# Optimization experiments

Measured on AMD Instinct MI355X. Metric: run time of the kernel, lower is better.

Reference implementation:

```python
import jax, jax.numpy as jnp
import numpy as np

EPS = 1e-5
NHEADS = 4
NLAYERS = 6

def layernorm(x, g, b):
    m = jnp.mean(x, axis=-1, keepdims=True)
    v = jnp.var(x, axis=-1, keepdims=True)
    return (x - m) * jax.lax.rsqrt(v + EPS) * g + b

def leaky_relu(x):
    return jnp.where(x >= 0, x, 0.1 * x)  # LeakyReLU(negative_slope=0.1)

def biased_mha(x, bias, mask, Wq, bq, Wk, bk, Wv, bv, Wo, bo):
    # dgl.nn.BiasedMHA: scores = (q/sqrt(dh)) k^T + bias (per-head), mask==True -> -inf
    B, N, D = x.shape
    dh = D // NHEADS
    q = (x @ Wq + bq).reshape(B, N, NHEADS, dh) * (dh ** -0.5)
    k = (x @ Wk + bk).reshape(B, N, NHEADS, dh)
    v = (x @ Wv + bv).reshape(B, N, NHEADS, dh)
    scores = jnp.einsum('bqhd,bkhd->bqkh', q, k) + bias  # [B,N,N,H]
    scores = jnp.where(mask[..., None], -jnp.inf, scores)
    w = jax.nn.softmax(scores, axis=2)  # softmax over keys
    out = jnp.einsum('bqkh,bkhd->bqhd', w, v).reshape(B, N, D)
    return out @ Wo + bo

def graphormer_forward(node_feat_new, attn_bias, deg_in_emb, deg_out_emb,
                       mlp_n_W1, mlp_n_b1, mlp_n_W2, mlp_n_b2,
                       Wq, bq, Wk, bk, Wv, bv, Wo, bo,
                       ln1_g, ln1_b, W1, b1, W2, b2, ln2_g, ln2_b,
                       mlp_out_W1, mlp_out_b1, mlp_out_W2, mlp_out_b2,
                       in_degree, out_degree, attn_mask, po_idx):
    # DegreeEncoder (directed): clamp to max_degree=8, sum of two embedding tables
    deg = deg_in_emb[jnp.clip(in_degree, 0, 8)] + deg_out_emb[jnp.clip(out_degree, 0, 8)]
    # mlp_n: Linear -> LeakyReLU(0.1) -> Linear
    h = leaky_relu(node_feat_new @ mlp_n_W1 + mlp_n_b1) @ mlp_n_W2 + mlp_n_b2
    x = h + deg
    mask = attn_mask != 0
    for i in range(NLAYERS):  # 6 GraphormerLayers, norm_first=False (post-norm)
        res = x
        a = biased_mha(x, attn_bias, mask, Wq[i], bq[i], Wk[i], bk[i], Wv[i], bv[i], Wo[i], bo[i])
        x = layernorm(res + a, ln1_g[i], ln1_b[i])
        res = x
        f = jax.nn.relu(x @ W1[i] + b1[i]) @ W2[i] + b2[i]  # FFN with ReLU
        x = layernorm(res + f, ln2_g[i], ln2_b[i])
    B = x.shape[0]
    sel = x[jnp.arange(B)[:, None], po_idx].reshape(-1, x.shape[-1])  # gather PO nodes
    return leaky_relu(sel @ mlp_out_W1 + mlp_out_b1) @ mlp_out_W2 + mlp_out_b2

def setup_inputs():
    B, N, F_IN, D, HID, P, L = 8, 1024, 64, 512, 1024, 128, 6
    key = jax.random.key(0)
    ks = jax.random.split(key, 32)
    def w(k, shape, fan_in):
        return jax.random.normal(k, shape, jnp.float32) / np.float32(np.sqrt(fan_in))
    return dict(
        node_feat_new=jax.random.normal(ks[0], (B, N, F_IN), jnp.float32),
        in_degree=jax.random.randint(ks[1], (B, N), 0, 9),
        out_degree=jax.random.randint(ks[2], (B, N), 0, 9),
        dist=jax.random.randint(ks[3], (B, N, N), 0, 6).astype(jnp.int32),
        attn_mask=jax.random.randint(ks[4], (B, N, N), 0, 2).astype(jnp.int32),
        po_idx=jax.random.randint(ks[5], (B, P), 0, N),
        attn_bias=jax.random.uniform(ks[6], (B, N, N, NHEADS), jnp.float32),
        deg_in_emb=w(ks[7], (9, D), D),
        deg_out_emb=w(ks[8], (9, D), D),
        mlp_n_W1=w(ks[9], (F_IN, D // 2), F_IN), mlp_n_b1=jnp.zeros((D // 2,), jnp.float32),
        mlp_n_W2=w(ks[10], (D // 2, D), D // 2), mlp_n_b2=jnp.zeros((D,), jnp.float32),
        Wq=w(ks[11], (L, D, D), D), bq=jnp.zeros((L, D), jnp.float32),
        Wk=w(ks[12], (L, D, D), D), bk=jnp.zeros((L, D), jnp.float32),
        Wv=w(ks[13], (L, D, D), D), bv=jnp.zeros((L, D), jnp.float32),
        Wo=w(ks[14], (L, D, D), D), bo=jnp.zeros((L, D), jnp.float32),
        ln1_g=jnp.ones((L, D), jnp.float32), ln1_b=jnp.zeros((L, D), jnp.float32),
        W1=w(ks[15], (L, D, HID), D), b1=jnp.zeros((L, HID), jnp.float32),
        W2=w(ks[16], (L, HID, D), HID), b2=jnp.zeros((L, D), jnp.float32),
        ln2_g=jnp.ones((L, D), jnp.float32), ln2_b=jnp.zeros((L, D), jnp.float32),
        mlp_out_W1=w(ks[17], (D, D // 2), D), mlp_out_b1=jnp.zeros((D // 2,), jnp.float32),
        mlp_out_W2=w(ks[18], (D // 2, 1), D // 2), mlp_out_b2=jnp.zeros((1,), jnp.float32),
    )

def reference(node_feat_new, in_degree, out_degree, dist, attn_mask, po_idx, attn_bias,
              deg_in_emb, deg_out_emb, mlp_n_W1, mlp_n_b1, mlp_n_W2, mlp_n_b2,
              Wq, bq, Wk, bk, Wv, bv, Wo, bo, ln1_g, ln1_b, W1, b1, W2, b2, ln2_g, ln2_b,
              mlp_out_W1, mlp_out_b1, mlp_out_W2, mlp_out_b2):
    del dist  # original computes spatial encoding from dist but overwrites attn_bias with rand (dead code)
    return graphormer_forward(node_feat_new, attn_bias, deg_in_emb, deg_out_emb,
                              mlp_n_W1, mlp_n_b1, mlp_n_W2, mlp_n_b2,
                              Wq, bq, Wk, bk, Wv, bv, Wo, bo,
                              ln1_g, ln1_b, W1, b1, W2, b2, ln2_g, ln2_b,
                              mlp_out_W1, mlp_out_b1, mlp_out_W2, mlp_out_b2,
                              in_degree, out_degree, attn_mask, po_idx)
```

## Files before the change

kernel.cpp:

```cpp
#include <hip/hip_runtime.h>

typedef unsigned short u16;
typedef unsigned int u32;
typedef short bf16x8 __attribute__((ext_vector_type(8)));
typedef float f32x4 __attribute__((ext_vector_type(4)));

__device__ __forceinline__ float us2f(u16 u) {
  union { unsigned int i; float f; } x; x.i = ((unsigned int)u) << 16; return x.f;
}
__device__ __forceinline__ u16 f2bf(float f) {
  union { float f; unsigned int i; } x; x.f = f;
  unsigned int i = x.i;
  return (u16)((i + 0x7FFFu + ((i >> 16) & 1u)) >> 16);
}
__device__ __forceinline__ int probe_f32(const void* p) {
  return ((const u16*)p)[0] == 0;
}
__device__ __forceinline__ float ldf(const void* p, size_t i, int f32) {
  return f32 ? ((const float*)p)[i] : us2f(((const u16*)p)[i]);
}
__device__ __forceinline__ float4 ldf4(const void* p, size_t i, int f32) {
  if (f32) return *(const float4*)((const float*)p + i);
  const ushort4 t = *(const ushort4*)((const u16*)p + i);
  return make_float4(us2f(t.x), us2f(t.y), us2f(t.z), us2f(t.w));
}

__global__ __launch_bounds__(256) void gemm_mfma(
    const void* __restrict__ probe, const void* __restrict__ A, int a_mode,
    int lda, const void* __restrict__ W, size_t wOff,
    const void* __restrict__ bias, size_t bOff, const u16* __restrict__ res,
    void* __restrict__ C, int c_bf16, int M, int N, int K, int act) {
  const int in_f32 = probe_f32(probe);
  const int a_f32 = (a_mode == 2) ? in_f32 : 0;
  __shared__ u16 As[2][128][40];
  __shared__ u16 Bt[2][64][40];
  const int tid = threadIdx.x;
  const int n0 = blockIdx.x * 64, m0 = blockIdx.y * 128;
  const int wv = tid >> 6, lane = tid & 63;
  const int lk = lane & 15, quad = lane >> 4;
  const int wm = wv * 32;

  f32x4 acc[2][4];
#pragma unroll
  for (int i = 0; i < 2; i++)
#pragma unroll
    for (int j = 0; j < 4; j++) acc[i][j] = (f32x4){0.f, 0.f, 0.f, 0.f};

  const int sar = tid >> 1, sac = (tid & 1) * 16;
  const int kp = tid & 15, nseg = tid >> 4;

  u16 abuf[16];
  u32 wbuf[8];
  auto loadA = [&](int k0) {
    if (a_f32) {
      const float* ap = (const float*)A + (size_t)(m0 + sar) * lda + k0 + sac;
#pragma unroll
      for (int q = 0; q < 4; q++) {
        const float4 f = *(const float4*)(ap + q * 4);
        abuf[q * 4 + 0] = f2bf(f.x); abuf[q * 4 + 1] = f2bf(f.y);
        abuf[q * 4 + 2] = f2bf(f.z); abuf[q * 4 + 3] = f2bf(f.w);
      }
    } else {
      const u16* ap = (const u16*)A + (size_t)(m0 + sar) * lda + k0 + sac;
      *(bf16x8*)&abuf[0] = *(const bf16x8*)ap;
      *(bf16x8*)&abuf[8] = *(const bf16x8*)(ap + 8);
    }
  };
  auto loadW = [&](int k0) {
    if (tid < 128) {
      const size_t wb = wOff + (size_t)(k0 + 2 * kp) * N + n0 + nseg * 8;
      if (in_f32) {
        const float* wp = (const float*)W + wb;
#pragma unroll
        for (int i = 0; i < 8; i++)
          wbuf[i] = ((u32)f2bf(wp[N + i]) << 16) | (u32)f2bf(wp[i]);
      } else {
        const u16* wp = (const u16*)W + wb;
#pragma unroll
        for (int i = 0; i < 8; i++)
          wbuf[i] = ((u32)wp[N + i] << 16) | (u32)wp[i];
      }
    }
  };
  auto store = [&](int bi) {
    *(bf16x8*)&As[bi][sar][sac] = *(bf16x8*)&abuf[0];
    *(bf16x8*)&As[bi][sar][sac + 8] = *(bf16x8*)&abuf[8];
    if (tid < 128) {
#pragma unroll
      for (int i = 0; i < 8; i++) *(u32*)&Bt[bi][nseg * 8 + i][2 * kp] = wbuf[i];
    }
  };

  const int nk = K >> 5;
  loadA(0); loadW(0); store(0);
  __syncthreads();
  for (int kt = 0; kt < nk; kt++) {
    const int cur = kt & 1;
    if (kt + 1 < nk) { loadA((kt + 1) * 32); loadW((kt + 1) * 32); }
    bf16x8 af[2], bfv[4];
#pragma unroll
    for (int i = 0; i < 2; i++)
      af[i] = *(const bf16x8*)&As[cur][wm + i * 16 + lk][quad * 8];
#pragma unroll
    for (int j = 0; j < 4; j++)
      bfv[j] = *(const bf16x8*)&Bt[cur][j * 16 + lk][quad * 8];
#pragma unroll
    for (int i = 0; i < 2; i++)
#pragma unroll
      for (int j = 0; j < 4; j++)
        acc[i][j] = __builtin_amdgcn_mfma_f32_16x16x32_bf16(af[i], bfv[j],
                                                            acc[i][j], 0, 0, 0);
    if (kt + 1 < nk) store(cur ^ 1);
    __syncthreads();
  }

#pragma unroll
  for (int j = 0; j < 4; j++) {
    const int col = n0 + j * 16 + lk;
    const float bb = bias ? ldf(bias, bOff + col, in_f32) : 0.f;
#pragma unroll
    for (int i = 0; i < 2; i++) {
#pragma unroll
      for (int r = 0; r < 4; r++) {
        const int row = m0 + wm + i * 16 + quad * 4 + r;
        float t = acc[i][j][r] + bb;
        if (act == 1) t = t > 0.f ? t : 0.f;
        else if (act == 2) t = t >= 0.f ? t : 0.1f * t;
        if (res) t += us2f(res[(size_t)row * N + col]);
        if (c_bf16) ((u16*)C)[(size_t)row * N + col] = f2bf(t);
        else ((float*)C)[(size_t)row * N + col] = t;
      }
    }
  }
}

__global__ __launch_bounds__(256) void gemm_qkv(
    const void* __restrict__ probe, const u16* __restrict__ A,
    const void* __restrict__ Wq, const void* __restrict__ Wk,
    const void* __restrict__ Wv, size_t wOff, const void* __restrict__ bq,
    const void* __restrict__ bk, const void* __restrict__ bv, size_t bOff,
    u16* __restrict__ C) {
  const int in_f32 = probe_f32(probe);
  __shared__ u16 As[2][128][40];
  __shared__ u16 Bt[2][64][40];
  const int tid = threadIdx.x;
  const int n0 = blockIdx.x * 64, m0 = blockIdx.y * 128;
  const int src = n0 >> 9, nn0 = n0 & 511;
  const void* W = src == 0 ? Wq : (src == 1 ? Wk : Wv);
  const void* bias = src == 0 ? bq : (src == 1 ? bk : bv);
  const int wv = tid >> 6, lane = tid & 63;
  const int lk = lane & 15, quad = lane >> 4;
  const int wm = wv * 32;

  f32x4 acc[2][4];
#pragma unroll
  for (int i = 0; i < 2; i++)
#pragma unroll
    for (int j = 0; j < 4; j++) acc[i][j] = (f32x4){0.f, 0.f, 0.f, 0.f};

  const int sar = tid >> 1, sac = (tid & 1) * 16;
  const int kp = tid & 15, nseg = tid >> 4;

  u16 abuf[16];
  u32 wbuf[8];
  auto loadA = [&](int k0) {
    const u16* ap = A + (size_t)(m0 + sar) * 512 + k0 + sac;
    *(bf16x8*)&abuf[0] = *(const bf16x8*)ap;
    *(bf16x8*)&abuf[8] = *(const bf16x8*)(ap + 8);
  };
  auto loadW = [&](int k0) {
    if (tid < 128) {
      const size_t wb = wOff + (size_t)(k0 + 2 * kp) * 512 + nn0 + nseg * 8;
      if (in_f32) {
        const float* wp = (const float*)W + wb;
#pragma unroll
        for (int i = 0; i < 8; i++)
          wbuf[i] = ((u32)f2bf(wp[512 + i]) << 16) | (u32)f2bf(wp[i]);
      } else {
        const u16* wp = (const u16*)W + wb;
#pragma unroll
        for (int i = 0; i < 8; i++)
          wbuf[i] = ((u32)wp[512 + i] << 16) | (u32)wp[i];
      }
    }
  };
  auto store = [&](int bi) {
    *(bf16x8*)&As[bi][sar][sac] = *(bf16x8*)&abuf[0];
    *(bf16x8*)&As[bi][sar][sac + 8] = *(bf16x8*)&abuf[8];
    if (tid < 128) {
#pragma unroll
      for (int i = 0; i < 8; i++) *(u32*)&Bt[bi][nseg * 8 + i][2 * kp] = wbuf[i];
    }
  };

  loadA(0); loadW(0); store(0);
  __syncthreads();
  for (int kt = 0; kt < 16; kt++) {
    const int cur = kt & 1;
    if (kt < 15) { loadA((kt + 1) * 32); loadW((kt + 1) * 32); }
    bf16x8 af[2], bfv[4];
#pragma unroll
    for (int i = 0; i < 2; i++)
      af[i] = *(const bf16x8*)&As[cur][wm + i * 16 + lk][quad * 8];
#pragma unroll
    for (int j = 0; j < 4; j++)
      bfv[j] = *(const bf16x8*)&Bt[cur][j * 16 + lk][quad * 8];
#pragma unroll
    for (int i = 0; i < 2; i++)
#pragma unroll
      for (int j = 0; j < 4; j++)
        acc[i][j] = __builtin_amdgcn_mfma_f32_16x16x32_bf16(af[i], bfv[j],
                                                            acc[i][j], 0, 0, 0);
    if (kt < 15) store(cur ^ 1);
    __syncthreads();
  }

#pragma unroll
  for (int j = 0; j < 4; j++) {
    const int coll = nn0 + j * 16 + lk;
    const float bb = ldf(bias, bOff + coll, in_f32);
#pragma unroll
    for (int i = 0; i < 2; i++) {
#pragma unroll
      for (int r = 0; r < 4; r++) {
        const int row = m0 + wm + i * 16 + quad * 4 + r;
        C[(size_t)row * 1536 + n0 + j * 16 + lk] = f2bf(acc[i][j][r] + bb);
      }
    }
  }
}

__global__ __launch_bounds__(256) void deg_kernel(const void* __restrict__ probe,
    u16* __restrict__ x, const int* __restrict__ ind, const int* __restrict__ outd,
    const void* __restrict__ ein, const void* __restrict__ eout) {
  const int f32 = probe_f32(probe);
  const int r = blockIdx.x, tid = threadIdx.x;
  int a = ind[r]; a = a < 0 ? 0 : (a > 8 ? 8 : a);
  int b = outd[r]; b = b < 0 ? 0 : (b > 8 ? 8 : b);
  const size_t base = (size_t)r * 512;
  for (int c = tid; c < 512; c += 256) {
    const float v = us2f(x[base + c]) + ldf(ein, (size_t)a * 512 + c, f32) +
                    ldf(eout, (size_t)b * 512 + c, f32);
    x[base + c] = f2bf(v);
  }
}

__global__ __launch_bounds__(256) void bias_pack(const void* __restrict__ probe,
    const void* __restrict__ bias, const int* __restrict__ mask,
    u16* __restrict__ biasm) {
  const int f32 = probe_f32(probe);
  const int bq = blockIdx.x;
  const int k = threadIdx.x * 4;
  const size_t rk = (size_t)bq * 1024 + k;
  const int4 mv = *(const int4*)(mask + rk);
  const float4 hk0 = ldf4(bias, rk * 4, f32);
  const float4 hk1 = ldf4(bias, rk * 4 + 4, f32);
  const float4 hk2 = ldf4(bias, rk * 4 + 8, f32);
  const float4 hk3 = ldf4(bias, rk * 4 + 12, f32);
  const u16 NB = f2bf(-3.0e38f);
  const int b = bq >> 10, q = bq & 1023;
  const size_t ob = (((size_t)b * 4 * 1024) + q) * 1024 + k;
#define PACK(H, C)                                                   \
  {                                                                  \
    ushort4 p;                                                       \
    p.x = mv.x ? NB : f2bf(hk0.C); p.y = mv.y ? NB : f2bf(hk1.C);    \
    p.z = mv.z ? NB : f2bf(hk2.C); p.w = mv.w ? NB : f2bf(hk3.C);    \
    *(ushort4*)(biasm + ob + ((size_t)H << 20)) = p;                 \
  }
  PACK(0, x)
  PACK(1, y)
  PACK(2, z)
  PACK(3, w)
#undef PACK
}

__global__ __launch_bounds__(256) void attn_mfma(const void* __restrict__ probe,
    const u16* __restrict__ QKV, const void* __restrict__ bias,
    const int* __restrict__ mask, u16* __restrict__ O,
    const u16* __restrict__ biasm) {
  const int f32 = probe_f32(probe);
  __shared__ u16 Kls[2][32][136];
  __shared__ u16 Vt[2][128][40];
  __shared__ u16 Pl[4][16][40];
  const int b = blockIdx.z, h = blockIdx.y, q0 = blockIdx.x * 64;
  const int tid = threadIdx.x;
  const int wv = tid >> 6, lane = tid & 63;
  const int lk = lane & 15, quad = lane >> 4;
  const float scale = 0.08838834764831845f;
  const float NEG = -3.0e38f;

  const size_t qg = (size_t)(b * 1024 + q0 + wv * 16);
  const int lq = q0 + wv * 16;
  const u16* bm = biasm ? biasm + (((size_t)(b * 4 + h)) << 20) : (const u16*)0;

  bf16x8 qf[4];
#pragma unroll
  for (int c = 0; c < 4; c++)
    qf[c] = *(const bf16x8*)(QKV + (qg + lk) * 1536 + h * 128 + c * 32 + quad * 8);

  f32x4 o[8];
#pragma unroll
  for (int c = 0; c < 8; c++) o[c] = (f32x4){0.f, 0.f, 0.f, 0.f};
  float m_st[4], l_st[4];
#pragma unroll
  for (int r = 0; r < 4; r++) { m_st[r] = NEG; l_st[r] = 0.f; }

  const int kp = tid & 15, dseg = tid >> 4;

  bf16x8 ka, kb2, va, vb2;
  auto loadKV = [&](int k0) {
    const size_t r0 = (size_t)(b * 1024 + k0 + 2 * kp) * 1536 + h * 128 + dseg * 8;
    ka  = *(const bf16x8*)(QKV + r0 + 512);
    kb2 = *(const bf16x8*)(QKV + r0 + 512 + 1536);
    va  = *(const bf16x8*)(QKV + r0 + 1024);
    vb2 = *(const bf16x8*)(QKV + r0 + 1024 + 1536);
  };
  auto storeKV = [&](int bi) {
    *(bf16x8*)&Kls[bi][2 * kp][dseg * 8] = ka;
    *(bf16x8*)&Kls[bi][2 * kp + 1][dseg * 8] = kb2;
#pragma unroll
    for (int i = 0; i < 8; i++) {
      const unsigned int pk =
          ((unsigned int)(u16)vb2[i] << 16) | (unsigned int)(u16)va[i];
      *(unsigned int*)&Vt[bi][dseg * 8 + i][2 * kp] = pk;
    }
  };

  loadKV(0); storeKV(0);
  __syncthreads();

  for (int kt = 0; kt < 32; kt++) {
    const int cur = kt & 1;
    const int k0 = kt * 32;
    if (kt < 31) loadKV((kt + 1) * 32);

    f32x4 sa[2];
#pragma unroll
    for (int kh = 0; kh < 2; kh++) {
      sa[kh] = (f32x4){0.f, 0.f, 0.f, 0.f};
#pragma unroll
      for (int c = 0; c < 4; c++) {
        const bf16x8 kf = *(const bf16x8*)&Kls[cur][kh * 16 + lk][c * 32 + quad * 8];
        sa[kh] = __builtin_amdgcn_mfma_f32_16x16x32_bf16(qf[c], kf, sa[kh], 0, 0, 0);
      }
    }
    float sv[2][4];
    if (bm) {
#pragma unroll
      for (int kh = 0; kh < 2; kh++)
#pragma unroll
        for (int r = 0; r < 4; r++)
          sv[kh][r] = sa[kh][r] * scale +
              us2f(bm[(size_t)(lq + quad * 4 + r) * 1024 + (k0 + kh * 16 + lk)]);
    } else {
#pragma unroll
      for (int kh = 0; kh < 2; kh++)
#pragma unroll
        for (int r = 0; r < 4; r++) {
          const size_t bidx = (qg + quad * 4 + r) * 1024 + (size_t)(k0 + kh * 16 + lk);
          const float s = sa[kh][r] * scale + ldf(bias, bidx * 4 + h, f32);
          sv[kh][r] = mask[bidx] ? NEG : s;
        }
    }
#pragma unroll
    for (int r = 0; r < 4; r++) {
      float lm = fmaxf(sv[0][r], sv[1][r]);
      lm = fmaxf(lm, __shfl_xor(lm, 1));
      lm = fmaxf(lm, __shfl_xor(lm, 2));
      lm = fmaxf(lm, __shfl_xor(lm, 4));
      lm = fmaxf(lm, __shfl_xor(lm, 8));
      const float mn = fmaxf(m_st[r], lm);
      const float al = __expf(m_st[r] - mn);
      const float p0 = (sv[0][r] <= -1e37f) ? 0.f : __expf(sv[0][r] - mn);
      const float p1 = (sv[1][r] <= -1e37f) ? 0.f : __expf(sv[1][r] - mn);
      float ts = p0 + p1;
      ts += __shfl_xor(ts, 1);
      ts += __shfl_xor(ts, 2);
      ts += __shfl_xor(ts, 4);
      ts += __shfl_xor(ts, 8);
      m_st[r] = mn;
      l_st[r] = l_st[r] * al + ts;
      Pl[wv][quad * 4 + r][lk] = f2bf(p0);
      Pl[wv][quad * 4 + r][16 + lk] = f2bf(p1);
#pragma unroll
      for (int c = 0; c < 8; c++) o[c][r] *= al;
    }
    const bf16x8 pa = *(const bf16x8*)&Pl[wv][lk][quad * 8];
#pragma unroll
    for (int c = 0; c < 8; c++) {
      const bf16x8 vf = *(const bf16x8*)&Vt[cur][c * 16 + lk][quad * 8];
      o[c] = __builtin_amdgcn_mfma_f32_16x16x32_bf16(pa, vf, o[c], 0, 0, 0);
    }
    if (kt < 31) storeKV(cur ^ 1);
    __syncthreads();
  }
#pragma unroll
  for (int r = 0; r < 4; r++) {
    const float invl = 1.f / fmaxf(l_st[r], 1e-20f);
    u16* op = O + (qg + quad * 4 + r) * 1536 + h * 128;
#pragma unroll
    for (int c = 0; c < 8; c++) op[c * 16 + lk] = f2bf(o[c][r] * invl);
  }
}

__global__ __launch_bounds__(256) void ln_kernel(const void* __restrict__ probe,
    const u16* __restrict__ in, const void* __restrict__ g,
    const void* __restrict__ bta, size_t gOff, u16* __restrict__ out) {
  const int f32 = probe_f32(probe);
  const int r = blockIdx.x, tid = threadIdx.x;
  const size_t base = (size_t)r * 512;
  const float a = us2f(in[base + tid]), b = us2f(in[base + tid + 256]);
  float s = a + b, sq = a * a + b * b;
#pragma unroll
  for (int off = 32; off > 0; off >>= 1) {
    s += __shfl_down(s, off);
    sq += __shfl_down(sq, off);
  }
  __shared__ float ss[4], sqs[4], stat[2];
  const int w = tid >> 6;
  if ((tid & 63) == 0) { ss[w] = s; sqs[w] = sq; }
  __syncthreads();
  if (tid == 0) {
    const float S = ss[0] + ss[1] + ss[2] + ss[3];
    const float SQ = sqs[0] + sqs[1] + sqs[2] + sqs[3];
    const float m = S * (1.f / 512.f);
    const float var = fmaxf(SQ * (1.f / 512.f) - m * m, 0.f);
    stat[0] = m; stat[1] = rsqrtf(var + 1e-5f);
  }
  __syncthreads();
  const float m = stat[0], rs = stat[1];
  out[base + tid] =
      f2bf((a - m) * rs * ldf(g, gOff + tid, f32) + ldf(bta, gOff + tid, f32));
  out[base + tid + 256] = f2bf((b - m) * rs * ldf(g, gOff + tid + 256, f32) +
                               ldf(bta, gOff + tid + 256, f32));
}

__global__ __launch_bounds__(256) void final_kernel(const void* __restrict__ probe,
    const u16* __restrict__ x, const int* __restrict__ po,
    const void* __restrict__ W1, const void* __restrict__ b1,
    const void* __restrict__ W2, const void* __restrict__ b2,
    void* __restrict__ out) {
  const int f32 = probe_f32(probe);
  __shared__ float rsr[512];
  __shared__ float red[256];
  const int r = blockIdx.x, tid = threadIdx.x;
  const int b = r >> 7, p = r & 127;
  int n = po[b * 128 + p]; n = n < 0 ? 0 : (n > 1023 ? 1023 : n);
  const u16* row = x + ((size_t)(b * 1024 + n)) * 512;
  rsr[tid] = us2f(row[tid]); rsr[tid + 256] = us2f(row[tid + 256]);
  __syncthreads();
  float t = ldf(b1, tid, f32);
  for (int k = 0; k < 512; k++) t += rsr[k] * ldf(W1, (size_t)k * 256 + tid, f32);
  t = t >= 0.f ? t : 0.1f * t;
  red[tid] = t * ldf(W2, tid, f32);
  __syncthreads();
  for (int off = 128; off > 0; off >>= 1) {
    if (tid < off) red[tid] += red[tid + off];
    __syncthreads();
  }
  if (tid == 0) {
    const float v = red[0] + ldf(b2, 0, f32);
    if (f32) ((float*)out)[r] = v; else ((u16*)out)[r] = f2bf(v);
  }
}

extern "C" void kernel_launch(void* const* d_in, const int* in_sizes, int n_in,
                              void* d_out, int out_size, void* d_ws, size_t ws_size,
                              hipStream_t stream) {
  (void)in_sizes; (void)out_size;
  const int D = 512, HID = 1024, L = 6;
  const int M = 8192;

  const int sh = (n_in >= 33) ? 0 : 1;
#define IN(k) d_in[(k) - (((k) >= 4) ? sh : 0)]
  const void* nf   = IN(0);
  const int* ind   = (const int*)IN(1);
  const int* outd  = (const int*)IN(2);
  const int* amask = (const int*)IN(4);
  const int* po    = (const int*)IN(5);
  const void* abias = IN(6);
  const void* ein  = IN(7);
  const void* eout = IN(8);
  const void* mnW1 = IN(9);  const void* mnb1 = IN(10);
  const void* mnW2 = IN(11); const void* mnb2 = IN(12);
  const void* Wq = IN(13); const void* bq = IN(14);
  const void* Wk = IN(15); const void* bk = IN(16);
  const void* Wv = IN(17); const void* bv = IN(18);
  const void* Wo = IN(19); const void* bo = IN(20);
  const void* ln1g = IN(21); const void* ln1b = IN(22);
  const void* W1 = IN(23); const void* b1 = IN(24);
  const void* W2 = IN(25); const void* b2 = IN(26);
  const void* ln2g = IN(27); const void* ln2b = IN(28);
  const void* oW1 = IN(29); const void* ob1 = IN(30);
  const void* oW2 = IN(31); const void* ob2 = IN(32);
#undef IN
  const void* probe = ln1g;

  char* wsb = (char*)d_ws;
  u16* x   = (u16*)wsb;
  u16* yb  = (u16*)(wsb + ((size_t)8 << 20));
  u16* qkv = (u16*)(wsb + ((size_t)16 << 20));
  u16* h1b = yb;
  u16* hidb = qkv;
  u16* biasm = (ws_size >= ((size_t)104 << 20))
                   ? (u16*)(wsb + ((size_t)40 << 20)) : (u16*)0;

  dim3 blk(256);
  if (biasm) bias_pack<<<8192, blk, 0, stream>>>(probe, abias, amask, biasm);
  gemm_mfma<<<dim3(4, M / 128), blk, 0, stream>>>(probe, nf, 2, 64, mnW1, 0, mnb1, 0, nullptr, h1b, 1, M, 256, 64, 2);
  gemm_mfma<<<dim3(8, M / 128), blk, 0, stream>>>(probe, h1b, 1, 256, mnW2, 0, mnb2, 0, nullptr, x, 1, M, D, 256, 0);
  deg_kernel<<<M, blk, 0, stream>>>(probe, x, ind, outd, ein, eout);

  for (int l = 0; l < L; l++) {
    const size_t wO = (size_t)l * D * D, bO = (size_t)l * D;
    const size_t w1O = (size_t)l * D * HID, b1O = (size_t)l * HID;
    gemm_qkv<<<dim3(24, M / 128), blk, 0, stream>>>(probe, x, Wq, Wk, Wv, wO, bq, bk, bv, bO, qkv);
    attn_mfma<<<dim3(16, 4, 8), blk, 0, stream>>>(probe, qkv, abias, amask, qkv, biasm);
    gemm_mfma<<<dim3(D / 64, M / 128), blk, 0, stream>>>(probe, qkv, 1, 1536, Wo, wO, bo, bO, x, yb, 1, M, D, D, 0);
    ln_kernel<<<M, blk, 0, stream>>>(probe, yb, ln1g, ln1b, bO, x);
    gemm_mfma<<<dim3(HID / 64, M / 128), blk, 0, stream>>>(probe, x, 1, 512, W1, w1O, b1, b1O, nullptr, hidb, 1, M, HID, D, 1);
    gemm_mfma<<<dim3(D / 64, M / 128), blk, 0, stream>>>(probe, hidb, 1, 1024, W2, w1O, b2, bO, x, yb, 1, M, D, HID, 0);
    ln_kernel<<<M, blk, 0, stream>>>(probe, yb, ln2g, ln2b, bO, x);
  }
  final_kernel<<<1024, blk, 0, stream>>>(probe, x, po, oW1, ob1, oW2, ob2, d_out);
}
```

Measured before the change: 1.938 ms.

## Widen GEMM N-tiles, make LayerNorm one wave per row, coalesce bias packing

The GEMM kernel is templated on the N tile width. The QKV and FFN1 GEMMs now use 128-wide tiles, so each block does more MFMA work per A-tile load and all 256 threads load weights. LayerNorm now assigns one wavefront per row, using vectorized 8-element loads and shuffle-only reductions, with no shared memory or block barriers. The bias_pack kernel stages per-head planes in LDS so it can write contiguous 16-byte stores instead of scattered 8-byte ones. Wider tiles double accumulator registers and halve the grid for those GEMMs, which may lower occupancy.

```diff
diff --git a/kernel.cpp b/kernel.cpp
--- a/kernel.cpp
+++ b/kernel.cpp
@@ -25,26 +25,28 @@
   return make_float4(us2f(t.x), us2f(t.y), us2f(t.z), us2f(t.w));
 }
 
-__global__ __launch_bounds__(256) void gemm_mfma(
+template <int BN>
+__global__ __launch_bounds__(256) void gemm_mfma_t(
     const void* __restrict__ probe, const void* __restrict__ A, int a_mode,
     int lda, const void* __restrict__ W, size_t wOff,
     const void* __restrict__ bias, size_t bOff, const u16* __restrict__ res,
     void* __restrict__ C, int c_bf16, int M, int N, int K, int act) {
   const int in_f32 = probe_f32(probe);
   const int a_f32 = (a_mode == 2) ? in_f32 : 0;
+  constexpr int NT = BN / 16;
   __shared__ u16 As[2][128][40];
-  __shared__ u16 Bt[2][64][40];
+  __shared__ u16 Bt[2][BN][40];
   const int tid = threadIdx.x;
-  const int n0 = blockIdx.x * 64, m0 = blockIdx.y * 128;
+  const int n0 = blockIdx.x * BN, m0 = blockIdx.y * 128;
   const int wv = tid >> 6, lane = tid & 63;
   const int lk = lane & 15, quad = lane >> 4;
   const int wm = wv * 32;
 
-  f32x4 acc[2][4];
+  f32x4 acc[2][NT];
 #pragma unroll
   for (int i = 0; i < 2; i++)
 #pragma unroll
-    for (int j = 0; j < 4; j++) acc[i][j] = (f32x4){0.f, 0.f, 0.f, 0.f};
+    for (int j = 0; j < NT; j++) acc[i][j] = (f32x4){0.f, 0.f, 0.f, 0.f};
 
   const int sar = tid >> 1, sac = (tid & 1) * 16;
   const int kp = tid & 15, nseg = tid >> 4;
@@ -67,7 +69,7 @@
     }
   };
   auto loadW = [&](int k0) {
-    if (tid < 128) {
+    if (BN == 128 || tid < 128) {
       const size_t wb = wOff + (size_t)(k0 + 2 * kp) * N + n0 + nseg * 8;
       if (in_f32) {
         const float* wp = (const float*)W + wb;
@@ -85,7 +87,7 @@
   auto store = [&](int bi) {
     *(bf16x8*)&As[bi][sar][sac] = *(bf16x8*)&abuf[0];
     *(bf16x8*)&As[bi][sar][sac + 8] = *(bf16x8*)&abuf[8];
-    if (tid < 128) {
+    if (BN == 128 || tid < 128) {
 #pragma unroll
       for (int i = 0; i < 8; i++) *(u32*)&Bt[bi][nseg * 8 + i][2 * kp] = wbuf[i];
     }
@@ -97,17 +99,17 @@
   for (int kt = 0; kt < nk; kt++) {
     const int cur = kt & 1;
     if (kt + 1 < nk) { loadA((kt + 1) * 32); loadW((kt + 1) * 32); }
-    bf16x8 af[2], bfv[4];
+    bf16x8 af[2], bfv[NT];
 #pragma unroll
     for (int i = 0; i < 2; i++)
       af[i] = *(const bf16x8*)&As[cur][wm + i * 16 + lk][quad * 8];
 #pragma unroll
-    for (int j = 0; j < 4; j++)
+    for (int j = 0; j < NT; j++)
       bfv[j] = *(const bf16x8*)&Bt[cur][j * 16 + lk][quad * 8];
 #pragma unroll
     for (int i = 0; i < 2; i++)
 #pragma unroll
-      for (int j = 0; j < 4; j++)
+      for (int j = 0; j < NT; j++)
         acc[i][j] = __builtin_amdgcn_mfma_f32_16x16x32_bf16(af[i], bfv[j],
                                                             acc[i][j], 0, 0, 0);
     if (kt + 1 < nk) store(cur ^ 1);
@@ -115,7 +117,7 @@
   }
 
 #pragma unroll
-  for (int j = 0; j < 4; j++) {
+  for (int j = 0; j < NT; j++) {
     const int col = n0 + j * 16 + lk;
     const float bb = bias ? ldf(bias, bOff + col, in_f32) : 0.f;
 #pragma unroll
@@ -142,9 +144,9 @@
     u16* __restrict__ C) {
   const int in_f32 = probe_f32(probe);
   __shared__ u16 As[2][128][40];
-  __shared__ u16 Bt[2][64][40];
+  __shared__ u16 Bt[2][128][40];
   const int tid = threadIdx.x;
-  const int n0 = blockIdx.x * 64, m0 = blockIdx.y * 128;
+  const int n0 = blockIdx.x * 128, m0 = blockIdx.y * 128;
   const int src = n0 >> 9, nn0 = n0 & 511;
   const void* W = src == 0 ? Wq : (src == 1 ? Wk : Wv);
   const void* bias = src == 0 ? bq : (src == 1 ? bk : bv);
@@ -152,11 +154,11 @@
   const int lk = lane & 15, quad = lane >> 4;
   const int wm = wv * 32;
 
-  f32x4 acc[2][4];
+  f32x4 acc[2][8];
 #pragma unroll
   for (int i = 0; i < 2; i++)
 #pragma unroll
-    for (int j = 0; j < 4; j++) acc[i][j] = (f32x4){0.f, 0.f, 0.f, 0.f};
+    for (int j = 0; j < 8; j++) acc[i][j] = (f32x4){0.f, 0.f, 0.f, 0.f};
 
   const int sar = tid >> 1, sac = (tid & 1) * 16;
   const int kp = tid & 15, nseg = tid >> 4;
@@ -169,28 +171,24 @@
     *(bf16x8*)&abuf[8] = *(const bf16x8*)(ap + 8);
   };
   auto loadW = [&](int k0) {
-    if (tid < 128) {
-      const size_t wb = wOff + (size_t)(k0 + 2 * kp) * 512 + nn0 + nseg * 8;
-      if (in_f32) {
-        const float* wp = (const float*)W + wb;
-#pragma unroll
-        for (int i = 0; i < 8; i++)
-          wbuf[i] = ((u32)f2bf(wp[512 + i]) << 16) | (u32)f2bf(wp[i]);
-      } else {
-        const u16* wp = (const u16*)W + wb;
-#pragma unroll
-        for (int i = 0; i < 8; i++)
-          wbuf[i] = ((u32)wp[512 + i] << 16) | (u32)wp[i];
-      }
+    const size_t wb = wOff + (size_t)(k0 + 2 * kp) * 512 + nn0 + nseg * 8;
+    if (in_f32) {
+      const float* wp = (const float*)W + wb;
+#pragma unroll
+      for (int i = 0; i < 8; i++)
+        wbuf[i] = ((u32)f2bf(wp[512 + i]) << 16) | (u32)f2bf(wp[i]);
+    } else {
+      const u16* wp = (const u16*)W + wb;
+#pragma unroll
+      for (int i = 0; i < 8; i++)
+        wbuf[i] = ((u32)wp[512 + i] << 16) | (u32)wp[i];
     }
   };
   auto store = [&](int bi) {
     *(bf16x8*)&As[bi][sar][sac] = *(bf16x8*)&abuf[0];
     *(bf16x8*)&As[bi][sar][sac + 8] = *(bf16x8*)&abuf[8];
-    if (tid < 128) {
-#pragma unroll
-      for (int i = 0; i < 8; i++) *(u32*)&Bt[bi][nseg * 8 + i][2 * kp] = wbuf[i];
-    }
+#pragma unroll
+    for (int i = 0; i < 8; i++) *(u32*)&Bt[bi][nseg * 8 + i][2 * kp] = wbuf[i];
   };
 
   loadA(0); loadW(0); store(0);
@@ -198,17 +196,17 @@
   for (int kt = 0; kt < 16; kt++) {
     const int cur = kt & 1;
     if (kt < 15) { loadA((kt + 1) * 32); loadW((kt + 1) * 32); }
-    bf16x8 af[2], bfv[4];
+    bf16x8 af[2], bfv[8];
 #pragma unroll
     for (int i = 0; i < 2; i++)
       af[i] = *(const bf16x8*)&As[cur][wm + i * 16 + lk][quad * 8];
 #pragma unroll
-    for (int j = 0; j < 4; j++)
+    for (int j = 0; j < 8; j++)
       bfv[j] = *(const bf16x8*)&Bt[cur][j * 16 + lk][quad * 8];
 #pragma unroll
     for (int i = 0; i < 2; i++)
 #pragma unroll
-      for (int j = 0; j < 4; j++)
+      for (int j = 0; j < 8; j++)
         acc[i][j] = __builtin_amdgcn_mfma_f32_16x16x32_bf16(af[i], bfv[j],
                                                             acc[i][j], 0, 0, 0);
     if (kt < 15) store(cur ^ 1);
@@ -216,7 +214,7 @@
   }
 
 #pragma unroll
-  for (int j = 0; j < 4; j++) {
+  for (int j = 0; j < 8; j++) {
     const int coll = nn0 + j * 16 + lk;
     const float bb = ldf(bias, bOff + coll, in_f32);
 #pragma unroll
@@ -249,29 +247,33 @@
     const void* __restrict__ bias, const int* __restrict__ mask,
     u16* __restrict__ biasm) {
   const int f32 = probe_f32(probe);
-  const int bq = blockIdx.x;
-  const int k = threadIdx.x * 4;
-  const size_t rk = (size_t)bq * 1024 + k;
-  const int4 mv = *(const int4*)(mask + rk);
-  const float4 hk0 = ldf4(bias, rk * 4, f32);
-  const float4 hk1 = ldf4(bias, rk * 4 + 4, f32);
-  const float4 hk2 = ldf4(bias, rk * 4 + 8, f32);
-  const float4 hk3 = ldf4(bias, rk * 4 + 12, f32);
+  __shared__ u16 pl[4][1032];
+  const int bq = blockIdx.x, t = threadIdx.x;
+  const size_t rk = (size_t)bq * 1024;
   const u16 NB = f2bf(-3.0e38f);
+#pragma unroll
+  for (int j = 0; j < 4; j++) {
+    const int k = t + j * 256;
+    const int mv = mask[rk + k];
+    float h0, h1, h2, h3;
+    if (f32) {
+      const float4 f = *(const float4*)((const float*)bias + (rk + k) * 4);
+      h0 = f.x; h1 = f.y; h2 = f.z; h3 = f.w;
+    } else {
+      const ushort4 u = *(const ushort4*)((const u16*)bias + (rk + k) * 4);
+      h0 = us2f(u.x); h1 = us2f(u.y); h2 = us2f(u.z); h3 = us2f(u.w);
+    }
+    pl[0][k] = mv ? NB : f2bf(h0);
+    pl[1][k] = mv ? NB : f2bf(h1);
+    pl[2][k] = mv ? NB : f2bf(h2);
+    pl[3][k] = mv ? NB : f2bf(h3);
+  }
+  __syncthreads();
   const int b = bq >> 10, q = bq & 1023;
-  const size_t ob = (((size_t)b * 4 * 1024) + q) * 1024 + k;
-#define PACK(H, C)                                                   \
-  {                                                                  \
-    ushort4 p;                                                       \
-    p.x = mv.x ? NB : f2bf(hk0.C); p.y = mv.y ? NB : f2bf(hk1.C);    \
-    p.z = mv.z ? NB : f2bf(hk2.C); p.w = mv.w ? NB : f2bf(hk3.C);    \
-    *(ushort4*)(biasm + ob + ((size_t)H << 20)) = p;                 \
-  }
-  PACK(0, x)
-  PACK(1, y)
-  PACK(2, z)
-  PACK(3, w)
-#undef PACK
+  const int p = t & 3, seg = t >> 2;
+  u16* dst = biasm + (((size_t)(b * 4 + p)) << 20) + (size_t)q * 1024 + seg * 16;
+  *(bf16x8*)dst = *(const bf16x8*)&pl[p][seg * 16];
+  *(bf16x8*)(dst + 8) = *(const bf16x8*)&pl[p][seg * 16 + 8];
 }
 
 __global__ __launch_bounds__(256) void attn_mfma(const void* __restrict__ probe,
@@ -407,32 +409,35 @@
     const u16* __restrict__ in, const void* __restrict__ g,
     const void* __restrict__ bta, size_t gOff, u16* __restrict__ out) {
   const int f32 = probe_f32(probe);
-  const int r = blockIdx.x, tid = threadIdx.x;
-  const size_t base = (size_t)r * 512;
-  const float a = us2f(in[base + tid]), b = us2f(in[base + tid + 256]);
-  float s = a + b, sq = a * a + b * b;
+  const int lane = threadIdx.x & 63, w = threadIdx.x >> 6;
+  const size_t r = (size_t)blockIdx.x * 4 + w;
+  const size_t base = r * 512 + lane * 8;
+  const bf16x8 v = *(const bf16x8*)(in + base);
+  float xv[8];
+  float s = 0.f, sq = 0.f;
+#pragma unroll
+  for (int i = 0; i < 8; i++) {
+    xv[i] = us2f((u16)v[i]);
+    s += xv[i]; sq += xv[i] * xv[i];
+  }
 #pragma unroll
   for (int off = 32; off > 0; off >>= 1) {
-    s += __shfl_down(s, off);
-    sq += __shfl_down(sq, off);
-  }
-  __shared__ float ss[4], sqs[4], stat[2];
-  const int w = tid >> 6;
-  if ((tid & 63) == 0) { ss[w] = s; sqs[w] = sq; }
-  __syncthreads();
-  if (tid == 0) {
-    const float S = ss[0] + ss[1] + ss[2] + ss[3];
-    const float SQ = sqs[0] + sqs[1] + sqs[2] + sqs[3];
-    const float m = S * (1.f / 512.f);
-    const float var = fmaxf(SQ * (1.f / 512.f) - m * m, 0.f);
-    stat[0] = m; stat[1] = rsqrtf(var + 1e-5f);
-  }
-  __syncthreads();
-  const float m = stat[0], rs = stat[1];
-  out[base + tid] =
-      f2bf((a - m) * rs * ldf(g, gOff + tid, f32) + ldf(bta, gOff + tid, f32));
-  out[base + tid + 256] = f2bf((b - m) * rs * ldf(g, gOff + tid + 256, f32) +
-                               ldf(bta, gOff + tid + 256, f32));
+    s += __shfl_xor(s, off);
+    sq += __shfl_xor(sq, off);
+  }
+  const float m = s * (1.f / 512.f);
+  const float var = fmaxf(sq * (1.f / 512.f) - m * m, 0.f);
+  const float rs = rsqrtf(var + 1e-5f);
+  const float4 g0 = ldf4(g, gOff + lane * 8, f32);
+  const float4 g1 = ldf4(g, gOff + lane * 8 + 4, f32);
+  const float4 b0 = ldf4(bta, gOff + lane * 8, f32);
+  const float4 b1 = ldf4(bta, gOff + lane * 8 + 4, f32);
+  const float gg[8] = {g0.x, g0.y, g0.z, g0.w, g1.x, g1.y, g1.z, g1.w};
+  const float bb[8] = {b0.x, b0.y, b0.z, b0.w, b1.x, b1.y, b1.z, b1.w};
+  bf16x8 ov;
+#pragma unroll
+  for (int i = 0; i < 8; i++) ov[i] = (short)f2bf((xv[i] - m) * rs * gg[i] + bb[i]);
+  *(bf16x8*)(out + base) = ov;
 }
 
 __global__ __launch_bounds__(256) void final_kernel(const void* __restrict__ probe,
@@ -507,20 +512,20 @@
 
   dim3 blk(256);
   if (biasm) bias_pack<<<8192, blk, 0, stream>>>(probe, abias, amask, biasm);
-  gemm_mfma<<<dim3(4, M / 128), blk, 0, stream>>>(probe, nf, 2, 64, mnW1, 0, mnb1, 0, nullptr, h1b, 1, M, 256, 64, 2);
-  gemm_mfma<<<dim3(8, M / 128), blk, 0, stream>>>(probe, h1b, 1, 256, mnW2, 0, mnb2, 0, nullptr, x, 1, M, D, 256, 0);
+  gemm_mfma_t<64><<<dim3(4, M / 128), blk, 0, stream>>>(probe, nf, 2, 64, mnW1, 0, mnb1, 0, nullptr, h1b, 1, M, 256, 64, 2);
+  gemm_mfma_t<64><<<dim3(8, M / 128), blk, 0, stream>>>(probe, h1b, 1, 256, mnW2, 0, mnb2, 0, nullptr, x, 1, M, D, 256, 0);
   deg_kernel<<<M, blk, 0, stream>>>(probe, x, ind, outd, ein, eout);
 
   for (int l = 0; l < L; l++) {
     const size_t wO = (size_t)l * D * D, bO = (size_t)l * D;
     const size_t w1O = (size_t)l * D * HID, b1O = (size_t)l * HID;
-    gemm_qkv<<<dim3(24, M / 128), blk, 0, stream>>>(probe, x, Wq, Wk, Wv, wO, bq, bk, bv, bO, qkv);
+    gemm_qkv<<<dim3(12, M / 128), blk, 0, stream>>>(probe, x, Wq, Wk, Wv, wO, bq, bk, bv, bO, qkv);
     attn_mfma<<<dim3(16, 4, 8), blk, 0, stream>>>(probe, qkv, abias, amask, qkv, biasm);
-    gemm_mfma<<<dim3(D / 64, M / 128), blk, 0, stream>>>(probe, qkv, 1, 1536, Wo, wO, bo, bO, x, yb, 1, M, D, D, 0);
-    ln_kernel<<<M, blk, 0, stream>>>(probe, yb, ln1g, ln1b, bO, x);
-    gemm_mfma<<<dim3(HID / 64, M / 128), blk, 0, stream>>>(probe, x, 1, 512, W1, w1O, b1, b1O, nullptr, hidb, 1, M, HID, D, 1);
-    gemm_mfma<<<dim3(D / 64, M / 128), blk, 0, stream>>>(probe, hidb, 1, 1024, W2, w1O, b2, bO, x, yb, 1, M, D, HID, 0);
-    ln_kernel<<<M, blk, 0, stream>>>(probe, yb, ln2g, ln2b, bO, x);
+    gemm_mfma_t<64><<<dim3(D / 64, M / 128), blk, 0, stream>>>(probe, qkv, 1, 1536, Wo, wO, bo, bO, x, yb, 1, M, D, D, 0);
+    ln_kernel<<<M / 4, blk, 0, stream>>>(probe, yb, ln1g, ln1b, bO, x);
+    gemm_mfma_t<128><<<dim3(HID / 128, M / 128), blk, 0, stream>>>(probe, x, 1, 512, W1, w1O, b1, b1O, nullptr, hidb, 1, M, HID, D, 1);
+    gemm_mfma_t<64><<<dim3(D / 64, M / 128), blk, 0, stream>>>(probe, hidb, 1, 1024, W2, w1O, b2, bO, x, yb, 1, M, D, HID, 0);
+    ln_kernel<<<M / 4, blk, 0, stream>>>(probe, yb, ln2g, ln2b, bO, x);
   }
   final_kernel<<<1024, blk, 0, stream>>>(probe, x, po, oW1, ob1, oW2, ob2, d_out);
 }
```

Result: faster. 1.854 ms (-4.4%).
